# Optimization experiments

Measured on AMD Instinct MI355X. Metric: run time of the kernel, lower is better.

Reference implementation:

```python
import jax, jax.numpy as jnp
import numpy as np

N, C_IN, T, V = 64, 64, 64, 25
C_OUT = 64
DK = DV = 16
NH = 8
DKH, DVH = DK // NH, DV // NH
KT = 9
EPS = 1e-5


def make_pe(channel, joint_num, time_len):
    # temporal positional encoding: position index = frame id, repeated per joint
    pos = np.repeat(np.arange(time_len), joint_num).astype(np.float32)[:, None]
    pe = np.zeros((time_len * joint_num, channel), np.float32)
    div = np.exp(np.arange(0, channel, 2).astype(np.float32) * -(np.log(10000.0) / channel))
    pe[:, 0::2] = np.sin(pos * div)
    pe[:, 1::2] = np.cos(pos * div)
    return jnp.asarray(pe.reshape(time_len, joint_num, channel).transpose(2, 0, 1)[None])  # (1,C,time,joint)


def setup_inputs():
    key = jax.random.key(0)
    ks = jax.random.split(key, 17)
    rn = lambda k, s, sc=0.05: jax.random.normal(k, s, jnp.float32) * sc
    return {
        'x': jax.random.normal(ks[0], (N, C_IN, T, V), jnp.float32),
        'pe': make_pe(C_IN, V, 64),
        'data_bn_g': 1.0 + rn(ks[1], (C_IN * V,)),
        'data_bn_b': rn(ks[2], (C_IN * V,)),
        'qkv_w': rn(ks[3], (3 * DK + DV, C_IN), 0.1),
        'qkv_b': rn(ks[4], (3 * DK + DV,)),
        'attn_w': rn(ks[5], (DV, DV), 0.1),
        'attn_b': rn(ks[6], (DV,)),
        'tcn_w': rn(ks[7], (C_OUT - DV, C_IN, KT, 1), 0.05),
        'tcn_b': rn(ks[8], (C_OUT - DV,)),
        'tcn_bn_g': 1.0 + rn(ks[9], (C_OUT - DV,)),
        'tcn_bn_b': rn(ks[10], (C_OUT - DV,)),
        'fc1_w': rn(ks[11], (C_OUT // 2, C_OUT), 0.1),
        'fc1_b': rn(ks[12], (C_OUT // 2,)),
        'fc2_w': rn(ks[13], (C_OUT, C_OUT // 2), 0.1),
        'fc2_b': rn(ks[14], (C_OUT,)),
        'bn_g': 1.0 + rn(ks[15], (C_OUT,)),
        'bn_b': rn(ks[16], (C_OUT,)),
    }


def _bn_eval(x, g, b, axis=1):
    # eval-mode BatchNorm with running_mean=0, running_var=1
    shape = [1] * x.ndim
    shape[axis] = -1
    scale = g / jnp.sqrt(1.0 + EPS)
    return x * scale.reshape(shape) + b.reshape(shape)


def _qkv_heads(x2d, qkv_w, qkv_b):
    # x2d: (B, C, T); 1x1 conv == channel matmul; split q/k/g/v, g is projected but unused
    qkv = jnp.einsum('oc,bct->bot', qkv_w, x2d) + qkv_b[None, :, None]
    q, k, _g, v = jnp.split(qkv, [DK, 2 * DK, 3 * DK], axis=1)
    B = x2d.shape[0]
    split = lambda z, ch: z.reshape(B, NH, ch // NH, -1)  # (B, Nh, chh, T)
    q = split(q, DK) * (DKH ** -0.5)
    return q, split(k, DK), split(v, DV)


def reference(x, pe, data_bn_g, data_bn_b, qkv_w, qkv_b, attn_w, attn_b,
              tcn_w, tcn_b, tcn_bn_g, tcn_bn_b, fc1_w, fc1_b, fc2_w, fc2_b, bn_g, bn_b):
    y = x + pe[:, :, :T]                                 # positional encoding (N,C,T,V)
    x_sum = x
    # data_bn over flattened (C*V) channels
    xb = x.transpose(0, 1, 3, 2).reshape(N, C_IN * V, T)
    xb = _bn_eval(xb, data_bn_g, data_bn_b)
    xn = xb.reshape(N, C_IN, V, T).transpose(0, 1, 3, 2)  # (N,C,T,V)
    # fold joints into batch: (N*V, C, T)
    xf = xn.transpose(0, 3, 1, 2).reshape(N * V, C_IN, T)
    yf = y.transpose(0, 3, 1, 2).reshape(N * V, C_IN, T)
    fq, fk, fv = _qkv_heads(xf, qkv_w, qkv_b)
    pq, pk, _ = _qkv_heads(yf, qkv_w, qkv_b)
    mu_q = fq.mean(-1, keepdims=True)                     # (B,H,dkh,1)
    fqc = fq - mu_q
    logits_pos = jnp.einsum('bhcs,bhct->bhst', pq, pk)    # (B,H,T,T)
    pairwise = jnp.einsum('bhcs,bhct->bhst', fqc, fk)     # (B,H,T,T)
    unary = jnp.einsum('bhcs,bhct->bhst', mu_q, fk)       # (B,H,1,T)
    weights = jnp.tanh(pairwise + logits_pos) + jnp.tanh(unary + logits_pos)
    ao = jnp.einsum('bhst,bhct->bhsc', weights, fv)       # (B,H,T,dvh)
    # (B,H,1,T,dvh) -> permute(0,1,4,2,3) -> combine heads -> (B, DV, T)
    ao = ao.transpose(0, 1, 3, 2).reshape(N * V, DV, T)
    ao = jnp.einsum('oc,bct->bot', attn_w, ao) + attn_b[None, :, None]
    ao = ao.reshape(N, V, DV, T).transpose(0, 2, 3, 1)    # (N, DV, T, V)
    # temporal conv branch (Unit2D: conv(k=9 temporal) + eval BN)
    tc = jax.lax.conv_general_dilated(x_sum, tcn_w, (1, 1), ((KT // 2, KT // 2), (0, 0)),
                                      dimension_numbers=('NCHW', 'OIHW', 'NCHW'))
    tc = tc + tcn_b[None, :, None, None]
    tc = _bn_eval(tc, tcn_bn_g, tcn_bn_b)
    result = jnp.concatenate([tc, ao], axis=1) + x_sum    # residual (down is None)
    # SE-style channel gating
    se = result.mean(axis=(2, 3))                         # (N, C_OUT)
    gate = jax.nn.sigmoid(jax.nn.relu(se @ fc1_w.T + fc1_b) @ fc2_w.T + fc2_b)
    result = result * gate[:, :, None, None] + result
    result = _bn_eval(result, bn_g, bn_b)
    return jax.nn.relu(result)
```

## Files before the change

kernel.cpp:

```cpp
#include <hip/hip_runtime.h>
#include <hip/hip_bf16.h>
#include <math.h>

#define TV_ 1600
#define SCALE_K 2.885390081777927f
#define RS2_ 0.70710678118654752f

typedef __attribute__((ext_vector_type(8))) short bf16x8;
typedef __attribute__((ext_vector_type(4))) float f32x4;
typedef __attribute__((ext_vector_type(2))) __fp16 h2f;

union F4H { float4 f; h2f h[4]; };
union F2H { float2 f; h2f h[2]; };

__device__ __forceinline__ float tanh4(float y) {
    float e = __builtin_amdgcn_exp2f(y);
    float r = __builtin_amdgcn_rcpf(e + 1.f);
    return __builtin_fmaf(-2.f, r, 1.f);
}

__device__ __forceinline__ float dot2f(h2f a, h2f b, float c) {
    return __builtin_amdgcn_fdot2(a, b, c, false);
}

__device__ __forceinline__ ushort f2bf(float f) {
    __hip_bfloat16 h = __float2bfloat16(f);
    return *(ushort*)&h;
}
__device__ __forceinline__ float bf2f(ushort u) {
    uint w = ((uint)u) << 16;
    return __uint_as_float(w);
}

__global__ __launch_bounds__(256) void t1_kernel(
    const float* __restrict__ x, const float* __restrict__ pe,
    const float* __restrict__ tcn_w, const float* __restrict__ tg,
    const float* __restrict__ qkv_w, const float* __restrict__ qkv_b,
    ushort* __restrict__ rt, float* __restrict__ Sp, float* __restrict__ Tt,
    ushort* __restrict__ wb, ushort* __restrict__ wq, float* __restrict__ qb,
    ushort* __restrict__ pet)
{
    const int tid = threadIdx.x;
    const int bx = blockIdx.x, by = blockIdx.y;

    if (bx == 25) {
        #pragma unroll 1
        for (int j = 0; j < 9; ++j) {
            int idx = by * 256 + tid + j * 16384;
            if (idx < 27648) {
                int oc = idx / 576, kk = idx - oc * 576;
                int kt = kk >> 6, ci = kk & 63;
                float a = tg[oc] * rsqrtf(1.f + 1e-5f);
                wb[idx] = f2bf(tcn_w[(oc * 64 + ci) * 9 + kt] * a);
            } else if (idx < 32768) {
                int i2 = idx - 27648;
                int r = i2 >> 6, c = i2 & 63;
                int src; float sc;
                if (r < 16)      { src = r;      sc = RS2_; }
                else if (r < 32) { src = r;      sc = SCALE_K; }
                else if (r < 48) { src = r + 16; sc = 1.f; }
                else if (r < 64) { src = r - 48; sc = RS2_; }
                else             { src = r - 48; sc = SCALE_K; }
                wq[i2] = f2bf(qkv_w[src * 64 + c] * sc);
            } else if (idx < 32848) {
                int r = idx - 32768;
                int src; float sc;
                if (r < 16)      { src = r;      sc = RS2_; }
                else if (r < 32) { src = r;      sc = SCALE_K; }
                else if (r < 48) { src = r + 16; sc = 1.f; }
                else if (r < 64) { src = r - 48; sc = RS2_; }
                else             { src = r - 48; sc = SCALE_K; }
                qb[r] = qkv_b[src] * sc;
            } else if (idx < 135248) {
                int i3 = idx - 32848;
                int ci = i3 / 1600, tv = i3 - ci * 1600;
                pet[tv * 64 + ci] = f2bf(pe[ci * 1600 + tv]);
            }
        }
        return;
    }
    if (bx == 26) {
        const int n = by;
        #pragma unroll
        for (int it = 0; it < 2; ++it) {
            int item = tid + it * 256;
            int ci = item >> 3, slot = item & 7;
            int t = (slot < 4) ? slot : (56 + slot);
            const float* xp = x + (n * 64 + ci) * TV_ + t * 25;
            float s = 0.f;
            #pragma unroll
            for (int v = 0; v < 25; ++v) s += xp[v];
            Tt[(n * 64 + ci) * 8 + slot] = s;
        }
        return;
    }

    __shared__ ushort smt[64 * 66];
    __shared__ float sps[64 * 65];
    const int tv0 = bx * 64;
    const int n = by;
    const int tvl = tid & 63, cig = tid >> 6;
    const int tv = tv0 + tvl;

    #pragma unroll
    for (int k = 0; k < 16; ++k) {
        int ci = cig * 16 + k;
        float xv = x[(n * 64 + ci) * TV_ + tv];
        smt[tvl * 66 + ci] = f2bf(xv);
        sps[ci * 65 + tvl] = xv;
    }
    __syncthreads();

    {
        const int c = tid >> 2, qr = tid & 3;
        float s = 0.f;
        #pragma unroll
        for (int i = 0; i < 16; ++i) s += sps[c * 65 + qr * 16 + i];
        s += __shfl_xor(s, 1);
        s += __shfl_xor(s, 2);
        if (qr == 0) Sp[(n * 25 + bx) * 64 + c] = s;
    }

    #pragma unroll
    for (int j = 0; j < 8; ++j) {
        int chunk = tid + j * 256;
        int tvr = chunk >> 5, p = chunk & 31;
        uint val = *(const uint*)&smt[tvr * 66 + p * 2];
        *(uint*)&rt[(n * TV_ + tv0 + tvr) * 64 + p * 2] = val;
    }
}

__global__ __launch_bounds__(256, 5) void score_kernel(
    const ushort* __restrict__ rt, const ushort* __restrict__ pet,
    const float* __restrict__ dbg, const float* __restrict__ dbb,
    const ushort* __restrict__ wq, const float* __restrict__ qb,
    const float* __restrict__ attn_w, const float* __restrict__ attn_b,
    float* __restrict__ aoc, float* __restrict__ sep)
{
    __shared__ float sm[5856];
    ushort* smu = (ushort*)sm;
    const int MU_ = 1056;
    const int FK2 = 1120, PK2 = 1664, FV2 = 2208, PQ2 = 2752, FQ2 = 3296;
    const int AO2 = 3840;
    const int UN_ = 5312;

    const int b = blockIdx.x;
    const int l = b >> 3;
    const int n = (b & 7) * 8 + l / 25;
    const int v = l % 25;
    const int tid = threadIdx.x;

    const int lane = tid & 63, wave = tid >> 6;
    const int m16 = lane & 15, q = lane >> 4;

    {
        const int part = tid & 7;
        const int ci0 = part * 8;
        const float rs = rsqrtf(1.f + 1e-5f);
        float sc8[8], sh8[8];
        #pragma unroll
        for (int i = 0; i < 8; ++i) {
            sc8[i] = dbg[(ci0 + i) * 25 + v] * rs;
            sh8[i] = dbb[(ci0 + i) * 25 + v];
        }
        #pragma unroll
        for (int j = 0; j < 2; ++j) {
            int t = (tid + j * 256) >> 3;
            uint4 xr = *(const uint4*)&rt[(n * TV_ + t * 25 + v) * 64 + ci0];
            uint4 pr = *(const uint4*)&pet[(t * 25 + v) * 64 + ci0];
            const ushort* xu = (const ushort*)&xr;
            const ushort* pu = (const ushort*)&pr;
            ushort xs[8], ys[8];
            #pragma unroll
            for (int i = 0; i < 8; ++i) {
                float xf = bf2f(xu[i]);
                xs[i] = f2bf(xf * sc8[i] + sh8[i]);
                ys[i] = f2bf(xf + bf2f(pu[i]));
            }
            *(uint4*)&smu[t * 72 + ci0] = *(uint4*)xs;
            *(uint4*)&smu[4608 + t * 72 + ci0] = *(uint4*)ys;
        }
    }
    __syncthreads();

    f32x4 acc[5];
    #pragma unroll
    for (int mt = 0; mt < 5; ++mt) acc[mt] = (f32x4){0.f, 0.f, 0.f, 0.f};
    #pragma unroll
    for (int kt = 0; kt < 2; ++kt) {
        const int koff = kt * 32 + q * 8;
        bf16x8 bx = *(const bf16x8*)&smu[(wave * 16 + m16) * 72 + koff];
        bf16x8 by = *(const bf16x8*)&smu[4608 + (wave * 16 + m16) * 72 + koff];
        #pragma unroll
        for (int mt = 0; mt < 5; ++mt) {
            bf16x8 a = *(const bf16x8*)&wq[(mt * 16 + m16) * 64 + koff];
            acc[mt] = __builtin_amdgcn_mfma_f32_16x16x32_bf16(a, (mt < 3) ? bx : by, acc[mt], 0, 0, 0);
        }
    }
    __syncthreads();

    {
        const int t = wave * 16 + m16;
        #pragma unroll
        for (int r = 0; r < 4; ++r)
            sm[(q * 4 + r) * 66 + t] = acc[0][r] + qb[q * 4 + r];
        const int p0 = (2 * q) * 68 + t, p1 = (2 * q + 1) * 68 + t;
        *(h2f*)&sm[FK2 + p0] = __builtin_amdgcn_cvt_pkrtz(acc[1][0] + qb[16 + 4 * q],     acc[1][1] + qb[16 + 4 * q + 1]);
        *(h2f*)&sm[FK2 + p1] = __builtin_amdgcn_cvt_pkrtz(acc[1][2] + qb[16 + 4 * q + 2], acc[1][3] + qb[16 + 4 * q + 3]);
        *(h2f*)&sm[FV2 + p0] = __builtin_amdgcn_cvt_pkrtz(acc[2][0] + qb[32 + 4 * q],     acc[2][1] + qb[32 + 4 * q + 1]);
        *(h2f*)&sm[FV2 + p1] = __builtin_amdgcn_cvt_pkrtz(acc[2][2] + qb[32 + 4 * q + 2], acc[2][3] + qb[32 + 4 * q + 3]);
        *(h2f*)&sm[PQ2 + p0] = __builtin_amdgcn_cvt_pkrtz(acc[3][0] + qb[48 + 4 * q],     acc[3][1] + qb[48 + 4 * q + 1]);
        *(h2f*)&sm[PQ2 + p1] = __builtin_amdgcn_cvt_pkrtz(acc[3][2] + qb[48 + 4 * q + 2], acc[3][3] + qb[48 + 4 * q + 3]);
        *(h2f*)&sm[PK2 + p0] = __builtin_amdgcn_cvt_pkrtz(acc[4][0] + qb[64 + 4 * q],     acc[4][1] + qb[64 + 4 * q + 1]);
        *(h2f*)&sm[PK2 + p1] = __builtin_amdgcn_cvt_pkrtz(acc[4][2] + qb[64 + 4 * q + 2], acc[4][3] + qb[64 + 4 * q + 3]);
    }
    __syncthreads();

    if (tid < 64) {
        int ch = tid & 15, qq = tid >> 4;
        float s = 0.f;
        #pragma unroll
        for (int t = 0; t < 16; ++t) s += sm[ch * 66 + qq * 16 + t];
        sm[MU_ + qq * 16 + ch] = s;
    }
    __syncthreads();
    if (tid < 16) {
        float mval = (sm[MU_ + tid] + sm[MU_ + 16 + tid] + sm[MU_ + 32 + tid] + sm[MU_ + 48 + tid]) * (1.f / 64.f);
        sm[MU_ + tid] = mval;
    }
    __syncthreads();

    #pragma unroll
    for (int e = 0; e < 2; ++e) {
        int idx = tid * 2 + e;
        int s = idx >> 3, h = idx & 7;
        float a = sm[(2 * h) * 66 + s] - sm[MU_ + 2 * h];
        float c = sm[(2 * h + 1) * 66 + s] - sm[MU_ + 2 * h + 1];
        *(h2f*)&sm[FQ2 + h * 68 + s] = __builtin_amdgcn_cvt_pkrtz(a, c);
    }
    {
        const int h = tid & 7, tt = tid >> 3;
        h2f mp = __builtin_amdgcn_cvt_pkrtz(sm[MU_ + 2 * h], sm[MU_ + 2 * h + 1]);
        sm[UN_ + h * 68 + tt]      = dot2f(mp, *(const h2f*)&sm[FK2 + h * 68 + tt], 0.f);
        sm[UN_ + h * 68 + tt + 32] = dot2f(mp, *(const h2f*)&sm[FK2 + h * 68 + tt + 32], 0.f);
    }
    __syncthreads();

    {
        const int h = tid & 7, sp = tid >> 3;
        const int hb = h * 68;
        F2H fqp, pqp;
        fqp.f = *(const float2*)&sm[FQ2 + hb + 2 * sp];
        pqp.f = *(const float2*)&sm[PQ2 + hb + 2 * sp];
        const h2f fq0 = fqp.h[0], fq1 = fqp.h[1];
        const h2f pq0 = pqp.h[0], pq1 = pqp.h[1];
        float ao00 = 0.f, ao01 = 0.f, ao10 = 0.f, ao11 = 0.f;
        #pragma unroll 2
        for (int t4 = 0; t4 < 16; ++t4) {
            F4H fk4, pk4, fv4;
            fk4.f = *(const float4*)&sm[FK2 + hb + 4 * t4];
            pk4.f = *(const float4*)&sm[PK2 + hb + 4 * t4];
            fv4.f = *(const float4*)&sm[FV2 + hb + 4 * t4];
            float4 un4 = *(const float4*)&sm[UN_ + hb + 4 * t4];
            const float* unp = (const float*)&un4;
            #pragma unroll
            for (int j = 0; j < 4; ++j) {
                float un = unp[j];
                float fva = (float)fv4.h[j].x, fvb = (float)fv4.h[j].y;
                float lp0 = dot2f(pq0, pk4.h[j], 0.f);
                float a10 = dot2f(fq0, fk4.h[j], lp0);
                float w0 = tanh4(a10) + tanh4(un + lp0);
                ao00 = __builtin_fmaf(w0, fva, ao00);
                ao01 = __builtin_fmaf(w0, fvb, ao01);
                float lp1 = dot2f(pq1, pk4.h[j], 0.f);
                float a11 = dot2f(fq1, fk4.h[j], lp1);
                float w1 = tanh4(a11) + tanh4(un + lp1);
                ao10 = __builtin_fmaf(w1, fva, ao10);
                ao11 = __builtin_fmaf(w1, fvb, ao11);
            }
        }
        *(float2*)&sm[AO2 + (2 * sp) * 20 + 2 * h]     = make_float2(ao00, ao01);
        *(float2*)&sm[AO2 + (2 * sp + 1) * 20 + 2 * h] = make_float2(ao10, ao11);
    }
    __syncthreads();

    const int t = tid & 63, oq = tid >> 6;
    float aorow[16];
    #pragma unroll
    for (int i = 0; i < 4; ++i)
        *(float4*)&aorow[i * 4] = *(const float4*)&sm[AO2 + t * 20 + i * 4];
    float* aop = aoc + (n * 25 + v) * 1024;
    #pragma unroll
    for (int j = 0; j < 4; ++j) {
        int o = oq * 4 + j;
        float acc4 = attn_b[o];
        #pragma unroll
        for (int c = 0; c < 16; ++c) acc4 += attn_w[o * 16 + c] * aorow[c];
        aop[o * 64 + t] = acc4;
        float ssum = acc4;
        #pragma unroll
        for (int off = 32; off >= 1; off >>= 1) ssum += __shfl_down(ssum, off, 64);
        if ((tid & 63) == 0) sep[(n * 25 + v) * 16 + o] = ssum;
    }
}

__global__ __launch_bounds__(512, 1) void tcn_mfma_kernel(
    const ushort* __restrict__ rt, const float* __restrict__ x,
    const ushort* __restrict__ wb,
    const float* __restrict__ tcn_b, const float* __restrict__ tg,
    const float* __restrict__ tb,
    const float* __restrict__ sep, const float* __restrict__ Sp,
    const float* __restrict__ Tt, const float* __restrict__ aoc,
    const float* __restrict__ fc1w, const float* __restrict__ fc1b,
    const float* __restrict__ fc2w, const float* __restrict__ fc2b,
    const float* __restrict__ bng, const float* __restrict__ bnb,
    float* __restrict__ out)
{
    __shared__ ushort xsl[600 * 72];
    __shared__ float U[576];
    __shared__ float gpart[432];
    __shared__ float SS[64], seL[64], hid[32], gateL[64];

    const int b = blockIdx.x;
    const int n = b >> 2, tile = b & 3;
    const int t0 = tile * 16;
    const int tid = threadIdx.x;
    const float rsbn = rsqrtf(1.f + 1e-5f);

    const int tvbase = (t0 - 4) * 25;
    for (int idx = tid; idx < 4800; idx += 512) {
        int r = idx >> 3, part = idx & 7;
        int tv = tvbase + r;
        uint4 val = make_uint4(0u, 0u, 0u, 0u);
        if (tv >= 0 && tv < TV_) val = *(const uint4*)&rt[(n * TV_ + tv) * 64 + part * 8];
        *(uint4*)&xsl[r * 72 + part * 8] = val;
    }

    if (tid < 64) {
        float S = 0.f;
        #pragma unroll 1
        for (int j = 0; j < 25; ++j) S += Sp[(n * 25 + j) * 64 + tid];
        SS[tid] = S;
        float T[8];
        #pragma unroll
        for (int j = 0; j < 8; ++j) T[j] = Tt[(n * 64 + tid) * 8 + j];
        U[tid * 9 + 0] = S - (T[4] + T[5] + T[6] + T[7]);
        U[tid * 9 + 1] = S - (T[5] + T[6] + T[7]);
        U[tid * 9 + 2] = S - (T[6] + T[7]);
        U[tid * 9 + 3] = S - T[7];
        U[tid * 9 + 4] = S;
        U[tid * 9 + 5] = S - T[0];
        U[tid * 9 + 6] = S - (T[0] + T[1]);
        U[tid * 9 + 7] = S - (T[0] + T[1] + T[2]);
        U[tid * 9 + 8] = S - (T[0] + T[1] + T[2] + T[3]);
    }
    __syncthreads();
    if (tid < 432) {
        int oc = tid / 9, kt = tid - oc * 9;
        float cs = 0.f;
        #pragma unroll
        for (int cb = 0; cb < 8; ++cb) {
            bf16x8 w8 = *(const bf16x8*)&wb[oc * 576 + kt * 64 + cb * 8];
            #pragma unroll
            for (int i = 0; i < 8; ++i)
                cs += bf2f((ushort)w8[i]) * U[(cb * 8 + i) * 9 + kt];
        }
        gpart[tid] = cs;
    }
    __syncthreads();
    if (tid < 64) {
        if (tid < 48) {
            float cs = 0.f;
            #pragma unroll
            for (int kt = 0; kt < 9; ++kt) cs += gpart[tid * 9 + kt];
            float a = tg[tid] * rsbn;
            float cb_ = tcn_b[tid] * a + tb[tid];
            seL[tid] = (a * cs + 1600.f * cb_ + SS[tid]) * (1.f / 1600.f);
        } else {
            float at = 0.f;
            #pragma unroll 1
            for (int j = 0; j < 25; ++j) at += sep[(n * 25 + j) * 16 + tid - 48];
            seL[tid] = (at + SS[tid]) * (1.f / 1600.f);
        }
    }
    __syncthreads();
    if (tid < 32) {
        float a = fc1b[tid];
        #pragma unroll
        for (int c = 0; c < 64; ++c) a += fc1w[tid * 64 + c] * seL[c];
        hid[tid] = fmaxf(a, 0.f);
    }
    __syncthreads();
    if (tid < 64) {
        float g = fc2b[tid];
        #pragma unroll
        for (int j = 0; j < 32; ++j) g += fc2w[tid * 32 + j] * hid[j];
        gateL[tid] = 1.f / (1.f + __expf(-g));
    }
    __syncthreads();

    const int lane = tid & 63, wave = tid >> 6;
    const int m16 = lane & 15, q = lane >> 4;
    const int nt0 = wave * 3;

    f32x4 acc[3][3];
    f32x4 acc24[3];
    #pragma unroll
    for (int i = 0; i < 3; ++i)
        #pragma unroll
        for (int mt = 0; mt < 3; ++mt)
            acc[i][mt] = (f32x4){0.f, 0.f, 0.f, 0.f};
    #pragma unroll
    for (int mt = 0; mt < 3; ++mt) acc24[mt] = (f32x4){0.f, 0.f, 0.f, 0.f};

    for (int ktile = 0; ktile < 18; ++ktile) {
        const int kt = ktile >> 1;
        const int cib = (ktile & 1) * 32 + q * 8;
        bf16x8 afr[3];
        #pragma unroll
        for (int mt = 0; mt < 3; ++mt)
            afr[mt] = *(const bf16x8*)&wb[(mt * 16 + m16) * 576 + ktile * 32 + q * 8];
        #pragma unroll
        for (int i = 0; i < 3; ++i) {
            int p = (nt0 + i) * 16 + m16;
            bf16x8 bfr = *(const bf16x8*)&xsl[(p + kt * 25) * 72 + cib];
            #pragma unroll
            for (int mt = 0; mt < 3; ++mt)
                acc[i][mt] = __builtin_amdgcn_mfma_f32_16x16x32_bf16(afr[mt], bfr, acc[i][mt], 0, 0, 0);
        }
        if (wave == 0) {
            int p = 24 * 16 + m16;
            bf16x8 bfr = *(const bf16x8*)&xsl[(p + kt * 25) * 72 + cib];
            #pragma unroll
            for (int mt = 0; mt < 3; ++mt)
                acc24[mt] = __builtin_amdgcn_mfma_f32_16x16x32_bf16(afr[mt], bfr, acc24[mt], 0, 0, 0);
        }
    }

    float cb3[3][4], m3_[3][4], bb3[3][4];
    #pragma unroll
    for (int mt = 0; mt < 3; ++mt)
        #pragma unroll
        for (int r = 0; r < 4; ++r) {
            int oc = mt * 16 + q * 4 + r;
            float a = tg[oc] * rsbn;
            cb3[mt][r] = tcn_b[oc] * a + tb[oc];
            m3_[mt][r] = (1.f + gateL[oc]) * (bng[oc] * rsbn);
            bb3[mt][r] = bnb[oc];
        }
    #pragma unroll
    for (int i = 0; i < 3; ++i) {
        int posg = tile * 400 + (nt0 + i) * 16 + m16;
        #pragma unroll
        for (int mt = 0; mt < 3; ++mt) {
            #pragma unroll
            for (int r = 0; r < 4; ++r) {
                int oc = mt * 16 + q * 4 + r;
                float val = acc[i][mt][r] + cb3[mt][r] + x[(n * 64 + oc) * TV_ + posg];
                out[(n * 64 + oc) * TV_ + posg] = fmaxf(val * m3_[mt][r] + bb3[mt][r], 0.f);
            }
        }
    }
    if (wave == 0) {
        int posg = tile * 400 + 24 * 16 + m16;
        #pragma unroll
        for (int mt = 0; mt < 3; ++mt) {
            #pragma unroll
            for (int r = 0; r < 4; ++r) {
                int oc = mt * 16 + q * 4 + r;
                float val = acc24[mt][r] + cb3[mt][r] + x[(n * 64 + oc) * TV_ + posg];
                out[(n * 64 + oc) * TV_ + posg] = fmaxf(val * m3_[mt][r] + bb3[mt][r], 0.f);
            }
        }
    }

    __syncthreads();
    float* ts = (float*)xsl;
    for (int task = tid; task < 1600; task += 512) {
        int v = task >> 6;
        int r = task & 63;
        int o = r >> 2, f = r & 3;
        float4 d = *(const float4*)&aoc[(n * 25 + v) * 1024 + o * 64 + tile * 16 + f * 4];
        float* dst = &ts[v * 257 + o * 16 + f * 4];
        dst[0] = d.x; dst[1] = d.y; dst[2] = d.z; dst[3] = d.w;
    }
    __syncthreads();
    for (int p4 = tid; p4 < 1600; p4 += 512) {
        int o = p4 / 100, r4 = p4 - o * 100;
        int base4 = (n * 64 + 48 + o) * 400 + tile * 100 + r4;
        float4 xr = ((const float4*)x)[base4];
        float4 val;
        #pragma unroll
        for (int e = 0; e < 4; ++e) {
            int pos = r4 * 4 + e;
            int lt = pos / 25, v = pos - lt * 25;
            ((float*)&val)[e] = ts[v * 257 + o * 16 + lt];
        }
        float mm = (1.f + gateL[48 + o]) * (bng[48 + o] * rsbn);
        float bb = bnb[48 + o];
        val.x = fmaxf((val.x + xr.x) * mm + bb, 0.f);
        val.y = fmaxf((val.y + xr.y) * mm + bb, 0.f);
        val.z = fmaxf((val.z + xr.z) * mm + bb, 0.f);
        val.w = fmaxf((val.w + xr.w) * mm + bb, 0.f);
        ((float4*)out)[base4] = val;
    }
}

extern "C" void kernel_launch(void* const* d_in, const int* in_sizes, int n_in,
                              void* d_out, int out_size, void* d_ws, size_t ws_size,
                              hipStream_t stream) {
    const float* x     = (const float*)d_in[0];
    const float* pe    = (const float*)d_in[1];
    const float* dbg   = (const float*)d_in[2];
    const float* dbb   = (const float*)d_in[3];
    const float* qkvw  = (const float*)d_in[4];
    const float* qkvb  = (const float*)d_in[5];
    const float* attnw = (const float*)d_in[6];
    const float* attnb = (const float*)d_in[7];
    const float* tcnw  = (const float*)d_in[8];
    const float* tcnb  = (const float*)d_in[9];
    const float* tcng  = (const float*)d_in[10];
    const float* tcnbb = (const float*)d_in[11];
    const float* fc1w  = (const float*)d_in[12];
    const float* fc1b  = (const float*)d_in[13];
    const float* fc2w  = (const float*)d_in[14];
    const float* fc2b  = (const float*)d_in[15];
    const float* bng   = (const float*)d_in[16];
    const float* bnb   = (const float*)d_in[17];

    float* out  = (float*)d_out;
    float* Sp   = (float*)d_ws;
    float* sep  = Sp + 102400;
    float* Tt   = sep + 25600;
    float* qb   = Tt + 32768;
    float* aoc  = qb + 96;
    ushort* wb  = (ushort*)(aoc + 1638400);
    ushort* wq  = wb + 27648;
    ushort* pet = wq + 5120;
    ushort* rt  = pet + 102400;

    t1_kernel<<<dim3(27, 64), dim3(256), 0, stream>>>(
        x, pe, tcnw, tcng, qkvw, qkvb, rt, Sp, Tt, wb, wq, qb, pet);
    score_kernel<<<dim3(1600), dim3(256), 0, stream>>>(rt, pet, dbg, dbb, wq, qb, attnw, attnb, aoc, sep);
    tcn_mfma_kernel<<<dim3(256), dim3(512), 0, stream>>>(
        rt, x, wb, tcnb, tcng, tcnbb, sep, Sp, Tt, aoc,
        fc1w, fc1b, fc2w, fc2b, bng, bnb, out);
}
```

Before: 192.0 us.

## Split SE gate into separate kernel and halve TCN shared-memory tile

```diff
diff --git a/kernel.cpp b/kernel.cpp
--- a/kernel.cpp
+++ b/kernel.cpp
@@ -304,43 +304,43 @@
     }
 }
 
-__global__ __launch_bounds__(512, 1) void tcn_mfma_kernel(
-    const ushort* __restrict__ rt, const float* __restrict__ x,
-    const ushort* __restrict__ wb,
+__global__ __launch_bounds__(256) void gate_kernel(
+    const float* __restrict__ Sp, const float* __restrict__ Tt,
+    const float* __restrict__ sep, const ushort* __restrict__ wb,
     const float* __restrict__ tcn_b, const float* __restrict__ tg,
     const float* __restrict__ tb,
-    const float* __restrict__ sep, const float* __restrict__ Sp,
-    const float* __restrict__ Tt, const float* __restrict__ aoc,
     const float* __restrict__ fc1w, const float* __restrict__ fc1b,
     const float* __restrict__ fc2w, const float* __restrict__ fc2b,
-    const float* __restrict__ bng, const float* __restrict__ bnb,
-    float* __restrict__ out)
+    float* __restrict__ gateG)
 {
-    __shared__ ushort xsl[600 * 72];
     __shared__ float U[576];
-    __shared__ float gpart[432];
-    __shared__ float SS[64], seL[64], hid[32], gateL[64];
-
-    const int b = blockIdx.x;
-    const int n = b >> 2, tile = b & 3;
-    const int t0 = tile * 16;
+    __shared__ float gp[432];
+    __shared__ float SS[64], sepS[16], seL[64], hid[32];
+    const int n = blockIdx.x;
     const int tid = threadIdx.x;
     const float rsbn = rsqrtf(1.f + 1e-5f);
 
-    const int tvbase = (t0 - 4) * 25;
-    for (int idx = tid; idx < 4800; idx += 512) {
-        int r = idx >> 3, part = idx & 7;
-        int tv = tvbase + r;
-        uint4 val = make_uint4(0u, 0u, 0u, 0u);
-        if (tv >= 0 && tv < TV_) val = *(const uint4*)&rt[(n * TV_ + tv) * 64 + part * 8];
-        *(uint4*)&xsl[r * 72 + part * 8] = val;
-    }
-
+    {
+        const int c = tid >> 2, qr = tid & 3;
+        float s = 0.f;
+        #pragma unroll 1
+        for (int j = qr; j < 25; j += 4) s += Sp[(n * 25 + j) * 64 + c];
+        s += __shfl_xor(s, 1);
+        s += __shfl_xor(s, 2);
+        if (qr == 0) SS[c] = s;
+    }
     if (tid < 64) {
-        float S = 0.f;
+        const int o = tid >> 2, qr = tid & 3;
+        float s = 0.f;
         #pragma unroll 1
-        for (int j = 0; j < 25; ++j) S += Sp[(n * 25 + j) * 64 + tid];
-        SS[tid] = S;
+        for (int j = qr; j < 25; j += 4) s += sep[(n * 25 + j) * 16 + o];
+        s += __shfl_xor(s, 1);
+        s += __shfl_xor(s, 2);
+        if (qr == 0) sepS[o] = s;
+    }
+    __syncthreads();
+    if (tid < 64) {
+        float S = SS[tid];
         float T[8];
         #pragma unroll
         for (int j = 0; j < 8; ++j) T[j] = Tt[(n * 64 + tid) * 8 + j];
@@ -365,22 +365,19 @@
             for (int i = 0; i < 8; ++i)
                 cs += bf2f((ushort)w8[i]) * U[(cb * 8 + i) * 9 + kt];
         }
-        gpart[tid] = cs;
+        gp[tid] = cs;
     }
     __syncthreads();
     if (tid < 64) {
         if (tid < 48) {
             float cs = 0.f;
             #pragma unroll
-            for (int kt = 0; kt < 9; ++kt) cs += gpart[tid * 9 + kt];
+            for (int kt = 0; kt < 9; ++kt) cs += gp[tid * 9 + kt];
             float a = tg[tid] * rsbn;
             float cb_ = tcn_b[tid] * a + tb[tid];
             seL[tid] = (a * cs + 1600.f * cb_ + SS[tid]) * (1.f / 1600.f);
         } else {
-            float at = 0.f;
-            #pragma unroll 1
-            for (int j = 0; j < 25; ++j) at += sep[(n * 25 + j) * 16 + tid - 48];
-            seL[tid] = (at + SS[tid]) * (1.f / 1600.f);
+            seL[tid] = (sepS[tid - 48] + SS[tid]) * (1.f / 1600.f);
         }
     }
     __syncthreads();
@@ -395,9 +392,30 @@
         float g = fc2b[tid];
         #pragma unroll
         for (int j = 0; j < 32; ++j) g += fc2w[tid * 32 + j] * hid[j];
-        gateL[tid] = 1.f / (1.f + __expf(-g));
-    }
-    __syncthreads();
+        gateG[n * 64 + tid] = 1.f / (1.f + __expf(-g));
+    }
+}
+
+__global__ __launch_bounds__(512, 4) void tcn_mfma_kernel(
+    const ushort* __restrict__ rt, const float* __restrict__ x,
+    const ushort* __restrict__ wb,
+    const float* __restrict__ tcn_b, const float* __restrict__ tg,
+    const float* __restrict__ tb,
+    const float* __restrict__ gateG, const float* __restrict__ aoc,
+    const float* __restrict__ bng, const float* __restrict__ bnb,
+    float* __restrict__ out)
+{
+    __shared__ ushort xsl[600 * 38];
+    __shared__ float gateL[64];
+
+    const int b = blockIdx.x;
+    const int n = b >> 2, tile = b & 3;
+    const int t0 = tile * 16;
+    const int tid = threadIdx.x;
+    const float rsbn = rsqrtf(1.f + 1e-5f);
+    const int tvbase = (t0 - 4) * 25;
+
+    if (tid < 64) gateL[tid] = gateG[n * 64 + tid];
 
     const int lane = tid & 63, wave = tid >> 6;
     const int m16 = lane & 15, q = lane >> 4;
@@ -413,63 +431,61 @@
     #pragma unroll
     for (int mt = 0; mt < 3; ++mt) acc24[mt] = (f32x4){0.f, 0.f, 0.f, 0.f};
 
-    for (int ktile = 0; ktile < 18; ++ktile) {
-        const int kt = ktile >> 1;
-        const int cib = (ktile & 1) * 32 + q * 8;
-        bf16x8 afr[3];
-        #pragma unroll
-        for (int mt = 0; mt < 3; ++mt)
-            afr[mt] = *(const bf16x8*)&wb[(mt * 16 + m16) * 576 + ktile * 32 + q * 8];
-        #pragma unroll
-        for (int i = 0; i < 3; ++i) {
-            int p = (nt0 + i) * 16 + m16;
-            bf16x8 bfr = *(const bf16x8*)&xsl[(p + kt * 25) * 72 + cib];
+    #pragma unroll 1
+    for (int hf = 0; hf < 2; ++hf) {
+        if (hf) __syncthreads();
+        for (int idx = tid; idx < 2400; idx += 512) {
+            int r = idx >> 2, part = idx & 3;
+            int tv = tvbase + r;
+            uint4 val = make_uint4(0u, 0u, 0u, 0u);
+            if (tv >= 0 && tv < TV_) val = *(const uint4*)&rt[(n * TV_ + tv) * 64 + hf * 32 + part * 8];
+            *(uint4*)&xsl[r * 38 + part * 8] = val;
+        }
+        __syncthreads();
+        #pragma unroll 1
+        for (int kt = 0; kt < 9; ++kt) {
+            const int ktile = kt * 2 + hf;
+            bf16x8 afr[3];
             #pragma unroll
             for (int mt = 0; mt < 3; ++mt)
-                acc[i][mt] = __builtin_amdgcn_mfma_f32_16x16x32_bf16(afr[mt], bfr, acc[i][mt], 0, 0, 0);
-        }
-        if (wave == 0) {
-            int p = 24 * 16 + m16;
-            bf16x8 bfr = *(const bf16x8*)&xsl[(p + kt * 25) * 72 + cib];
-            #pragma unroll
-            for (int mt = 0; mt < 3; ++mt)
-                acc24[mt] = __builtin_amdgcn_mfma_f32_16x16x32_bf16(afr[mt], bfr, acc24[mt], 0, 0, 0);
-        }
-    }
-
-    float cb3[3][4], m3_[3][4], bb3[3][4];
-    #pragma unroll
-    for (int mt = 0; mt < 3; ++mt)
+                afr[mt] = *(const bf16x8*)&wb[(mt * 16 + m16) * 576 + ktile * 32 + q * 8];
+            #pragma unroll
+            for (int i = 0; i < 3; ++i) {
+                int p = (nt0 + i) * 16 + m16;
+                bf16x8 bfr = *(const bf16x8*)&xsl[(p + kt * 25) * 38 + q * 8];
+                #pragma unroll
+                for (int mt = 0; mt < 3; ++mt)
+                    acc[i][mt] = __builtin_amdgcn_mfma_f32_16x16x32_bf16(afr[mt], bfr, acc[i][mt], 0, 0, 0);
+            }
+            if (wave == 0) {
+                int p = 24 * 16 + m16;
+                bf16x8 bfr = *(const bf16x8*)&xsl[(p + kt * 25) * 38 + q * 8];
+                #pragma unroll
+                for (int mt = 0; mt < 3; ++mt)
+                    acc24[mt] = __builtin_amdgcn_mfma_f32_16x16x32_bf16(afr[mt], bfr, acc24[mt], 0, 0, 0);
+            }
+        }
+    }
+
+    #pragma unroll
+    for (int mt = 0; mt < 3; ++mt) {
         #pragma unroll
         for (int r = 0; r < 4; ++r) {
             int oc = mt * 16 + q * 4 + r;
             float a = tg[oc] * rsbn;
-            cb3[mt][r] = tcn_b[oc] * a + tb[oc];
-            m3_[mt][r] = (1.f + gateL[oc]) * (bng[oc] * rsbn);
-            bb3[mt][r] = bnb[oc];
-        }
-    #pragma unroll
-    for (int i = 0; i < 3; ++i) {
-        int posg = tile * 400 + (nt0 + i) * 16 + m16;
-        #pragma unroll
-        for (int mt = 0; mt < 3; ++mt) {
-            #pragma unroll
-            for (int r = 0; r < 4; ++r) {
-                int oc = mt * 16 + q * 4 + r;
-                float val = acc[i][mt][r] + cb3[mt][r] + x[(n * 64 + oc) * TV_ + posg];
-                out[(n * 64 + oc) * TV_ + posg] = fmaxf(val * m3_[mt][r] + bb3[mt][r], 0.f);
-            }
-        }
-    }
-    if (wave == 0) {
-        int posg = tile * 400 + 24 * 16 + m16;
-        #pragma unroll
-        for (int mt = 0; mt < 3; ++mt) {
-            #pragma unroll
-            for (int r = 0; r < 4; ++r) {
-                int oc = mt * 16 + q * 4 + r;
-                float val = acc24[mt][r] + cb3[mt][r] + x[(n * 64 + oc) * TV_ + posg];
-                out[(n * 64 + oc) * TV_ + posg] = fmaxf(val * m3_[mt][r] + bb3[mt][r], 0.f);
+            float cb_ = tcn_b[oc] * a + tb[oc];
+            float mm = (1.f + gateL[oc]) * (bng[oc] * rsbn);
+            float bb = bnb[oc];
+            #pragma unroll
+            for (int i = 0; i < 3; ++i) {
+                int posg = tile * 400 + (nt0 + i) * 16 + m16;
+                float val = acc[i][mt][r] + cb_ + x[(n * 64 + oc) * TV_ + posg];
+                out[(n * 64 + oc) * TV_ + posg] = fmaxf(val * mm + bb, 0.f);
+            }
+            if (wave == 0) {
+                int posg = tile * 400 + 24 * 16 + m16;
+                float val = acc24[mt][r] + cb_ + x[(n * 64 + oc) * TV_ + posg];
+                out[(n * 64 + oc) * TV_ + posg] = fmaxf(val * mm + bb, 0.f);
             }
         }
     }
@@ -538,11 +554,13 @@
     ushort* wq  = wb + 27648;
     ushort* pet = wq + 5120;
     ushort* rt  = pet + 102400;
+    float* gateG = (float*)(rt + 6553600);
 
     t1_kernel<<<dim3(27, 64), dim3(256), 0, stream>>>(
         x, pe, tcnw, tcng, qkvw, qkvb, rt, Sp, Tt, wb, wq, qb, pet);
     score_kernel<<<dim3(1600), dim3(256), 0, stream>>>(rt, pet, dbg, dbb, wq, qb, attnw, attnb, aoc, sep);
+    gate_kernel<<<dim3(64), dim3(256), 0, stream>>>(
+        Sp, Tt, sep, wb, tcnb, tcng, tcnbb, fc1w, fc1b, fc2w, fc2b, gateG);
     tcn_mfma_kernel<<<dim3(256), dim3(512), 0, stream>>>(
-        rt, x, wb, tcnb, tcng, tcnbb, sep, Sp, Tt, aoc,
-        fc1w, fc1b, fc2w, fc2b, bng, bnb, out);
-}
+        rt, x, wb, tcnb, tcng, tcnbb, gateG, aoc, bng, bnb, out);
+}
```

After: 190.1 us. Within noise of the previous version (-1.0%).
